# Kernel optimization log

Measured on AMD Instinct MI355X. Metric: run time of the kernel, lower is better.

## Reference

```python
import jax, jax.numpy as jnp
import numpy as np

N_NODES = 50000
N_EDGES = 800000
R = 3          # relations
D_IN = 96
D_HID = 96
D_OUT = 64


def setup_inputs() -> dict:
    key = jax.random.key(0)
    ks = jax.random.split(key, 10)
    s_in = 1.0 / np.sqrt(D_IN)
    s_hid = 1.0 / np.sqrt(D_HID)
    return {
        "x": jax.random.normal(ks[0], (N_NODES, D_IN), jnp.float32),
        "src": jax.random.randint(ks[1], (R, N_EDGES), 0, N_NODES, jnp.int32),
        "dst": jax.random.randint(ks[2], (R, N_EDGES), 0, N_NODES, jnp.int32),
        "Ws1": jax.random.normal(ks[3], (R, D_IN, D_HID), jnp.float32) * s_in,
        "Wn1": jax.random.normal(ks[4], (R, D_IN, D_HID), jnp.float32) * s_in,
        "b1": jnp.zeros((R, D_HID), jnp.float32),
        "Ws2": jax.random.normal(ks[5], (R, D_HID, D_OUT), jnp.float32) * s_hid,
        "Wn2": jax.random.normal(ks[6], (R, D_HID, D_OUT), jnp.float32) * s_hid,
        "b2": jnp.zeros((R, D_OUT), jnp.float32),
    }


def reference(x, src, dst, Ws1, Wn1, b1, Ws2, Wn2, b2):
    N = x.shape[0]
    # in-degree per relation, clamped to 1 (DGL zero-in-degree convention)
    deg = jax.vmap(lambda d: jax.ops.segment_sum(
        jnp.ones(d.shape[0], x.dtype), d, num_segments=N))(dst)        # [R, N]
    inv_deg = (1.0 / jnp.maximum(deg, 1.0))[..., None]                 # [R, N, 1]

    def sage_layer(h, Ws, Wn, b):
        # gather src feats, mean-aggregate onto dst, per relation
        neigh = jax.vmap(lambda s, d: jax.ops.segment_sum(
            h[s], d, num_segments=N))(src, dst) * inv_deg              # [R, N, Din]
        out = jnp.tanh(
            jnp.einsum('nd,rdh->rnh', h, Ws)
            + jnp.einsum('rnd,rdh->rnh', neigh, Wn)
            + b[:, None, :])                                           # [R, N, H]
        return out.mean(axis=0)  # HeteroGraphConv aggregate='mean'

    h1 = sage_layer(x, Ws1, Wn1, b1)
    return sage_layer(h1, Ws2, Wn2, b2)
```

## Files before the change

kernel.cpp:

```cpp
#include <hip/hip_runtime.h>
#include <hip/hip_bf16.h>

constexpr int NN   = 50000;
constexpr int NE   = 800000;
constexpr int NR   = 3;
constexpr int DIN  = 96;
constexpr int DH   = 96;
constexpr int DOUT = 64;
constexpr int SLOT = 48;
constexpr int ZROW = NN;

constexpr float QS_X   = 127.0f / 5.5f;
constexpr float STEP_X = 5.5f / 127.0f;
constexpr float STEP_H = 1.0f / 127.0f;

constexpr int NBUCK   = 196;
constexpr int LCAP    = 56;
constexpr int P1B     = 256;
constexpr int CHUNK   = NE / P1B;
constexpr int BSTRIDE = 3200;
constexpr int LSTRIDE = 200;

constexpr int SCAT_BLKS = NR * P1B;
constexpr int CONV_BLKS = (NN * 96 + 4095) / 4096;
constexpr int WT_ELEMS  = 2 * NR * DIN * DH + 2 * NR * DH * DOUT;
constexpr int WT_BLKS   = (WT_ELEMS + 511) / 512;
constexpr int PREP_GRID = SCAT_BLKS + CONV_BLKS + WT_BLKS;

typedef __attribute__((ext_vector_type(8))) short bf16x8;
typedef __attribute__((ext_vector_type(4))) float f32x4;
typedef __attribute__((ext_vector_type(4))) unsigned int uint4v;

__device__ __forceinline__ unsigned short f2b(float f) {
    unsigned int u = __float_as_uint(f);
    u += 0x7fffu + ((u >> 16) & 1u);
    return (unsigned short)(u >> 16);
}
__device__ __forceinline__ unsigned int pack2(float lo, float hi) {
    return (unsigned int)f2b(lo) | ((unsigned int)f2b(hi) << 16);
}
__device__ __forceinline__ unsigned int q8u(float f, float s) {
    int v = (int)lrintf(f * s);
    v = v < -127 ? -127 : (v > 127 ? 127 : v);
    return (unsigned int)(v + 128);
}

struct __align__(4) U3 { unsigned int x, y, z; };

__global__ __launch_bounds__(512)
void prep_kernel(const int* __restrict__ src,
                 const int* __restrict__ dst,
                 unsigned int* __restrict__ gbuck,
                 int* __restrict__ glofs,
                 const float* __restrict__ x,
                 unsigned short* __restrict__ xb,
                 unsigned char* __restrict__ xq,
                 const float* __restrict__ Ws1, const float* __restrict__ Wn1,
                 const float* __restrict__ Ws2, const float* __restrict__ Wn2,
                 unsigned short* __restrict__ wt)
{
    __shared__ unsigned int lbuf[NBUCK][LCAP];
    __shared__ int lcnt[NBUCK];
    __shared__ int sa[256], sb[256];
    __shared__ int lofs[NBUCK + 1];

    const int bid = blockIdx.x;
    const int tid = threadIdx.x;

    if (bid < SCAT_BLKS) {
        const int r = bid >> 8, c = bid & 255;
        for (int i = tid; i < NBUCK; i += 512) lcnt[i] = 0;
        __syncthreads();

        const int* sr = src + (size_t)r * NE + (size_t)c * CHUNK;
        const int* dr = dst + (size_t)r * NE + (size_t)c * CHUNK;
        for (int i = tid; i < CHUNK; i += 512) {
            int d = dr[i];
            int s = sr[i];
            int b = d >> 8;
            int pos = atomicAdd(&lcnt[b], 1);
            if (pos < LCAP)
                lbuf[b][pos] = ((unsigned int)(d & 255) << 16) | (unsigned int)s;
        }
        __syncthreads();

        if (tid < 256)
            sa[tid] = (tid < NBUCK) ? min(lcnt[tid], LCAP) : 0;
        __syncthreads();
        int* cur = sa; int* nxt = sb;
        for (int st = 1; st < 256; st <<= 1) {
            if (tid < 256) {
                int v = cur[tid];
                if (tid >= st) v += cur[tid - st];
                nxt[tid] = v;
            }
            __syncthreads();
            int* t2 = cur; cur = nxt; nxt = t2;
        }
        if (tid == 0) lofs[0] = 0;
        if (tid < NBUCK) lofs[tid + 1] = cur[tid];
        __syncthreads();

        if (tid < NBUCK + 1) glofs[(size_t)bid * LSTRIDE + tid] = lofs[tid];

        const int w = tid >> 6, l = tid & 63;
        unsigned int* gb = gbuck + (size_t)bid * BSTRIDE;
        for (int b = w; b < NBUCK; b += 8) {
            int cnt = min(lcnt[b], LCAP);
            if (l < cnt) gb[lofs[b] + l] = lbuf[b][l];
        }
    } else if (bid < SCAT_BLKS + CONV_BLKS) {
        const int rb = bid - SCAT_BLKS;
        if (rb == 0) {
            if (tid < 48) {
                unsigned int* z = reinterpret_cast<unsigned int*>(xb + (size_t)ZROW * 96);
                z[tid] = 0u;
            } else if (tid >= 64 && tid < 88) {
                reinterpret_cast<unsigned int*>(xq + (size_t)ZROW * 96)[tid - 64] = 0x80808080u;
            }
        }
        int i = (rb * 512 + tid) * 8;
        if (i < NN * 96) {
            float4 a = *reinterpret_cast<const float4*>(x + i);
            float4 b = *reinterpret_cast<const float4*>(x + i + 4);
            uint4 o;
            o.x = pack2(a.x, a.y);
            o.y = pack2(a.z, a.w);
            o.z = pack2(b.x, b.y);
            o.w = pack2(b.z, b.w);
            *reinterpret_cast<uint4*>(xb + i) = o;
            unsigned int qlo = q8u(a.x, QS_X) | (q8u(a.y, QS_X) << 8)
                             | (q8u(a.z, QS_X) << 16) | (q8u(a.w, QS_X) << 24);
            unsigned int qhi = q8u(b.x, QS_X) | (q8u(b.y, QS_X) << 8)
                             | (q8u(b.z, QS_X) << 16) | (q8u(b.w, QS_X) << 24);
            unsigned int* q = reinterpret_cast<unsigned int*>(xq + i);
            q[0] = qlo;
            q[1] = qhi;
        }
    } else {
        int g = (bid - SCAT_BLKS - CONV_BLKS) * 512 + tid;
        if (g < WT_ELEMS) {
            constexpr int SZ1 = NR * DIN * DH;
            constexpr int SZ2 = NR * DH * DOUT;
            const float* in;
            int idx, KD, ND;
            if (g < SZ1)                { in = Ws1; idx = g;                 KD = DIN; ND = DH; }
            else if (g < 2 * SZ1)       { in = Wn1; idx = g - SZ1;           KD = DIN; ND = DH; }
            else if (g < 2 * SZ1 + SZ2) { in = Ws2; idx = g - 2 * SZ1;       KD = DH;  ND = DOUT; }
            else                        { in = Wn2; idx = g - 2 * SZ1 - SZ2; KD = DH;  ND = DOUT; }
            int k = idx % KD;
            int rn = idx / KD;
            int n = rn % ND;
            int r = rn / ND;
            wt[g] = f2b(in[((size_t)r * KD + k) * ND + n]);
        }
    }
}

__global__ __launch_bounds__(512)
void bin_build_kernel(const unsigned int* __restrict__ gbuck,
                      const int* __restrict__ glofs,
                      unsigned short* __restrict__ slots,
                      int* __restrict__ deg)
{
    __shared__ unsigned short lslot[256][SLOT];
    __shared__ int lcnt[256];

    const int rb = blockIdx.x;
    const int r  = rb / NBUCK, b = rb - r * NBUCK;
    const int nbase = b * 256;
    int nb = NN - nbase; if (nb > 256) nb = 256;
    const int tid = threadIdx.x;

    unsigned int* ls32i = reinterpret_cast<unsigned int*>(&lslot[0][0]);
    for (int i = tid; i < 256 * SLOT / 2; i += 512) ls32i[i] = 0xC350C350u;
    for (int i = tid; i < 256; i += 512) lcnt[i] = 0;
    __syncthreads();

    const int blk  = tid >> 1;
    const int half = tid & 1;
    const int gblk = r * P1B + blk;
    int o0 = glofs[(size_t)gblk * LSTRIDE + b];
    int o1 = glofs[(size_t)gblk * LSTRIDE + b + 1];
    const unsigned int* run = gbuck + (size_t)gblk * BSTRIDE + o0;
    int cnt = o1 - o0;
    for (int i = half; i < cnt; i += 2) {
        unsigned int e = run[i];
        int nl = e >> 16;
        int pos = atomicAdd(&lcnt[nl], 1);
        if (pos < SLOT) lslot[nl][pos] = (unsigned short)(e & 0xffffu);
    }
    __syncthreads();

    for (int j = tid; j < nb; j += 512) deg[r * NN + nbase + j] = lcnt[j];

    const unsigned int* ls32 = reinterpret_cast<const unsigned int*>(&lslot[0][0]);
    unsigned int* gs32 = reinterpret_cast<unsigned int*>(
        slots + ((size_t)r * NN + nbase) * SLOT);
    const int tot = nb * (SLOT / 2);
    for (int i = tid; i < tot; i += 512) gs32[i] = ls32[i];
}

__global__ __launch_bounds__(256)
void agg_q8_kernel(const unsigned char* __restrict__ Hq,
                   const unsigned short* __restrict__ slots,
                   const int* __restrict__ deg,
                   unsigned int* __restrict__ aggb,
                   float step)
{
    int gid = blockIdx.x * 256 + threadIdx.x;
    int grp = gid >> 3, t = gid & 7;
    if (grp >= NR * NN) return;
    const uint4v* sl4 = reinterpret_cast<const uint4v*>(slots + (size_t)grp * SLOT);
    int e = deg[grp];
    if (e > SLOT) e = SLOT;

    uint4v iv0 = __builtin_nontemporal_load(sl4 + 0);
    uint4v iv1 = __builtin_nontemporal_load(sl4 + 1);
    uint4v iv2 = __builtin_nontemporal_load(sl4 + 2);
    uint4v iv3 = __builtin_nontemporal_load(sl4 + 3);

    const unsigned char* Tb = Hq + 12 * t;
    unsigned int l0 = 0, h0 = 0, l1 = 0, h1 = 0, l2 = 0, h2 = 0;
    const unsigned int M = 0x00FF00FFu;

#define DO8Q(V)                                                                \
    {                                                                          \
        unsigned int i0 = (V).x & 0xffffu, i1 = (V).x >> 16;                   \
        unsigned int i2 = (V).y & 0xffffu, i3 = (V).y >> 16;                   \
        unsigned int i4 = (V).z & 0xffffu, i5 = (V).z >> 16;                   \
        unsigned int i6 = (V).w & 0xffffu, i7 = (V).w >> 16;                   \
        U3 g0 = *reinterpret_cast<const U3*>(Tb + (size_t)i0 * 96);            \
        U3 g1 = *reinterpret_cast<const U3*>(Tb + (size_t)i1 * 96);            \
        U3 g2 = *reinterpret_cast<const U3*>(Tb + (size_t)i2 * 96);            \
        U3 g3 = *reinterpret_cast<const U3*>(Tb + (size_t)i3 * 96);            \
        U3 g4 = *reinterpret_cast<const U3*>(Tb + (size_t)i4 * 96);            \
        U3 g5 = *reinterpret_cast<const U3*>(Tb + (size_t)i5 * 96);            \
        U3 g6 = *reinterpret_cast<const U3*>(Tb + (size_t)i6 * 96);            \
        U3 g7 = *reinterpret_cast<const U3*>(Tb + (size_t)i7 * 96);            \
        l0 += g0.x & M; h0 += (g0.x >> 8) & M;                                 \
        l1 += g0.y & M; h1 += (g0.y >> 8) & M;                                 \
        l2 += g0.z & M; h2 += (g0.z >> 8) & M;                                 \
        l0 += g1.x & M; h0 += (g1.x >> 8) & M;                                 \
        l1 += g1.y & M; h1 += (g1.y >> 8) & M;                                 \
        l2 += g1.z & M; h2 += (g1.z >> 8) & M;                                 \
        l0 += g2.x & M; h0 += (g2.x >> 8) & M;                                 \
        l1 += g2.y & M; h1 += (g2.y >> 8) & M;                                 \
        l2 += g2.z & M; h2 += (g2.z >> 8) & M;                                 \
        l0 += g3.x & M; h0 += (g3.x >> 8) & M;                                 \
        l1 += g3.y & M; h1 += (g3.y >> 8) & M;                                 \
        l2 += g3.z & M; h2 += (g3.z >> 8) & M;                                 \
        l0 += g4.x & M; h0 += (g4.x >> 8) & M;                                 \
        l1 += g4.y & M; h1 += (g4.y >> 8) & M;                                 \
        l2 += g4.z & M; h2 += (g4.z >> 8) & M;                                 \
        l0 += g5.x & M; h0 += (g5.x >> 8) & M;                                 \
        l1 += g5.y & M; h1 += (g5.y >> 8) & M;                                 \
        l2 += g5.z & M; h2 += (g5.z >> 8) & M;                                 \
        l0 += g6.x & M; h0 += (g6.x >> 8) & M;                                 \
        l1 += g6.y & M; h1 += (g6.y >> 8) & M;                                 \
        l2 += g6.z & M; h2 += (g6.z >> 8) & M;                                 \
        l0 += g7.x & M; h0 += (g7.x >> 8) & M;                                 \
        l1 += g7.y & M; h1 += (g7.y >> 8) & M;                                 \
        l2 += g7.z & M; h2 += (g7.z >> 8) & M;                                 \
    }

    int nb8 = (e + 7) >> 3;
    if (nb8 > 0) DO8Q(iv0);
    if (nb8 > 1) DO8Q(iv1);
    if (nb8 > 2) DO8Q(iv2);
    if (nb8 > 3) DO8Q(iv3);
    for (int i = 32; i < e; i += 8) {
        uint4v v = __builtin_nontemporal_load(sl4 + (i >> 3));
        DO8Q(v);
    }
#undef DO8Q

    const int bias = 128 * 8 * nb8;
    const float inv = step / (float)(e > 0 ? e : 1);
    float f0  = (float)((int)(l0 & 0xFFFFu) - bias) * inv;
    float f1  = (float)((int)(h0 & 0xFFFFu) - bias) * inv;
    float f2  = (float)((int)(l0 >> 16)     - bias) * inv;
    float f3  = (float)((int)(h0 >> 16)     - bias) * inv;
    float f4  = (float)((int)(l1 & 0xFFFFu) - bias) * inv;
    float f5  = (float)((int)(h1 & 0xFFFFu) - bias) * inv;
    float f6  = (float)((int)(l1 >> 16)     - bias) * inv;
    float f7  = (float)((int)(h1 >> 16)     - bias) * inv;
    float f8  = (float)((int)(l2 & 0xFFFFu) - bias) * inv;
    float f9  = (float)((int)(h2 & 0xFFFFu) - bias) * inv;
    float f10 = (float)((int)(l2 >> 16)     - bias) * inv;
    float f11 = (float)((int)(h2 >> 16)     - bias) * inv;

    unsigned int* o = aggb + (size_t)grp * 48 + t * 6;
    o[0] = pack2(f0, f1);
    o[1] = pack2(f2, f3);
    o[2] = pack2(f4, f5);
    o[3] = pack2(f6, f7);
    o[4] = pack2(f8, f9);
    o[5] = pack2(f10, f11);
}

template <int NOUT, bool OUT16>
__global__ __launch_bounds__(256)
void mfma_layer_kernel(const unsigned short* Hb,
                       const unsigned short* __restrict__ aggb,
                       const unsigned short* __restrict__ Wts,
                       const unsigned short* __restrict__ Wtn,
                       const float* __restrict__ bias,
                       unsigned short* o16,
                       unsigned char* oq8,
                       float* __restrict__ o32)
{
    const int w    = threadIdx.x >> 6;
    const int l    = threadIdx.x & 63;
    const int n0   = blockIdx.x * 64 + w * 16;
    const int arow = l & 15, asel = l >> 4;
    int na = n0 + arow;
    if (na > NN - 1) na = NN - 1;

    bf16x8 ax[3], ag[NR][3];
    {
        const unsigned short* xr = Hb + (size_t)na * 96 + asel * 8;
        #pragma unroll
        for (int kb = 0; kb < 3; ++kb)
            ax[kb] = *reinterpret_cast<const bf16x8*>(xr + kb * 32);
        #pragma unroll
        for (int r = 0; r < NR; ++r) {
            const unsigned short* gr = aggb + ((size_t)r * NN + na) * 96 + asel * 8;
            #pragma unroll
            for (int kb = 0; kb < 3; ++kb)
                ag[r][kb] = *reinterpret_cast<const bf16x8*>(gr + kb * 32);
        }
    }

    constexpr int NC = NOUT / 16;
    #pragma unroll
    for (int c = 0; c < NC; ++c) {
        f32x4 acc[NR];
        #pragma unroll
        for (int r = 0; r < NR; ++r) acc[r] = (f32x4){0.f, 0.f, 0.f, 0.f};

        #pragma unroll
        for (int r = 0; r < NR; ++r) {
            const unsigned short* bs = Wts + ((size_t)r * NOUT + c * 16 + arow) * 96 + asel * 8;
            const unsigned short* bn = Wtn + ((size_t)r * NOUT + c * 16 + arow) * 96 + asel * 8;
            #pragma unroll
            for (int kb = 0; kb < 3; ++kb) {
                acc[r] = __builtin_amdgcn_mfma_f32_16x16x32_bf16(
                    ax[kb], *reinterpret_cast<const bf16x8*>(bs + kb * 32), acc[r], 0, 0, 0);
                acc[r] = __builtin_amdgcn_mfma_f32_16x16x32_bf16(
                    ag[r][kb], *reinterpret_cast<const bf16x8*>(bn + kb * 32), acc[r], 0, 0, 0);
            }
        }

        const int col = c * 16 + arow;
        const float b0 = bias[col];
        const float b1 = bias[NOUT + col];
        const float b2 = bias[2 * NOUT + col];
        #pragma unroll
        for (int j = 0; j < 4; ++j) {
            int node = n0 + asel * 4 + j;
            if (node < NN) {
                float v = (tanhf(acc[0][j] + b0) + tanhf(acc[1][j] + b1)
                         + tanhf(acc[2][j] + b2)) * (1.0f / 3.0f);
                if (OUT16) {
                    o16[(size_t)node * 96 + col] = f2b(v);
                    oq8[(size_t)node * 96 + col] = (unsigned char)q8u(v, 127.0f);
                } else {
                    o32[(size_t)node * DOUT + col] = v;
                }
            }
        }
    }
}

extern "C" void kernel_launch(void* const* d_in, const int* in_sizes, int n_in,
                              void* d_out, int out_size, void* d_ws, size_t ws_size,
                              hipStream_t stream)
{
    const float* x   = (const float*)d_in[0];
    const int*   src = (const int*)d_in[1];
    const int*   dst = (const int*)d_in[2];
    const float* Ws1 = (const float*)d_in[3];
    const float* Wn1 = (const float*)d_in[4];
    const float* b1  = (const float*)d_in[5];
    const float* Ws2 = (const float*)d_in[6];
    const float* Wn2 = (const float*)d_in[7];
    const float* b2  = (const float*)d_in[8];
    float* out = (float*)d_out;

    char* ws = (char*)d_ws;
    size_t o = 0;
    auto alloc = [&](size_t bytes) {
        size_t p = o;
        o += (bytes + 255) & ~(size_t)255;
        return p;
    };
    int* deg = (int*)(ws + alloc((size_t)NR * NN * 4));
    unsigned short* slots = (unsigned short*)(ws + alloc((size_t)NR * NN * SLOT * 2));
    unsigned short* xb = (unsigned short*)(ws + alloc((size_t)(NN + 1) * 96 * 2));
    unsigned char* xq = (unsigned char*)(ws + alloc((size_t)(NN + 1) * 96));
    char* aggregion = ws + alloc((size_t)NR * NN * 96 * 2);
    unsigned short* wt = (unsigned short*)(ws + alloc((size_t)WT_ELEMS * 2));
    unsigned short* wt1s = wt;
    unsigned short* wt1n = wt1s + NR * DIN * DH;
    unsigned short* wt2s = wt1n + NR * DIN * DH;
    unsigned short* wt2n = wt2s + NR * DH * DOUT;

    unsigned int* gbuck = (unsigned int*)aggregion;
    int* glofs = (int*)(aggregion + (size_t)NR * P1B * BSTRIDE * 4);
    unsigned short* aggb = (unsigned short*)aggregion;

    prep_kernel<<<PREP_GRID, 512, 0, stream>>>(
        src, dst, gbuck, glofs, x, xb, xq, Ws1, Wn1, Ws2, Wn2, wt);
    bin_build_kernel<<<NR * NBUCK, 512, 0, stream>>>(gbuck, glofs, slots, deg);

    constexpr int AGG_GRID  = (NR * NN * 8 + 255) / 256;
    constexpr int GEMM_GRID = (NN + 63) / 64;

    agg_q8_kernel<<<AGG_GRID, 256, 0, stream>>>(
        xq, slots, deg, (unsigned int*)aggb, STEP_X);
    mfma_layer_kernel<DH, true><<<GEMM_GRID, 256, 0, stream>>>(
        xb, aggb, wt1s, wt1n, b1, xb, xq, (float*)nullptr);

    agg_q8_kernel<<<AGG_GRID, 256, 0, stream>>>(
        xq, slots, deg, (unsigned int*)aggb, STEP_H);
    mfma_layer_kernel<DOUT, false><<<GEMM_GRID, 256, 0, stream>>>(
        xb, aggb, wt2s, wt2n, b2, (unsigned short*)nullptr, (unsigned char*)nullptr, out);
}
```

Baseline: 171.3 us.

## Split GEMM layer kernels across output column blocks with separate hidden buffers

The dense layer kernels now launch several blocks per 64-node tile, each computing a subset of output column chunks, which raises the number of blocks in flight. Because blocks of the first layer can no longer safely overwrite the input features in place, the hidden activations are written to new bf16 and int8 buffers, and the zero padding row is initialised for them. The cost is that every column block reloads the same input and aggregated rows, multiplying A-side memory traffic unless it hits in cache.

```diff
diff --git a/kernel.cpp b/kernel.cpp
--- a/kernel.cpp
+++ b/kernel.cpp
@@ -55,6 +55,8 @@
                  const float* __restrict__ x,
                  unsigned short* __restrict__ xb,
                  unsigned char* __restrict__ xq,
+                 unsigned short* __restrict__ h1b,
+                 unsigned char* __restrict__ h1q,
                  const float* __restrict__ Ws1, const float* __restrict__ Wn1,
                  const float* __restrict__ Ws2, const float* __restrict__ Wn2,
                  unsigned short* __restrict__ wt)
@@ -113,10 +115,13 @@
         const int rb = bid - SCAT_BLKS;
         if (rb == 0) {
             if (tid < 48) {
-                unsigned int* z = reinterpret_cast<unsigned int*>(xb + (size_t)ZROW * 96);
-                z[tid] = 0u;
-            } else if (tid >= 64 && tid < 88) {
-                reinterpret_cast<unsigned int*>(xq + (size_t)ZROW * 96)[tid - 64] = 0x80808080u;
+                reinterpret_cast<unsigned int*>(xb  + (size_t)ZROW * 96)[tid] = 0u;
+            } else if (tid >= 64 && tid < 112) {
+                reinterpret_cast<unsigned int*>(h1b + (size_t)ZROW * 96)[tid - 64] = 0u;
+            } else if (tid >= 128 && tid < 152) {
+                reinterpret_cast<unsigned int*>(xq  + (size_t)ZROW * 96)[tid - 128] = 0x80808080u;
+            } else if (tid >= 192 && tid < 216) {
+                reinterpret_cast<unsigned int*>(h1q + (size_t)ZROW * 96)[tid - 192] = 0x80808080u;
             }
         }
         int i = (rb * 512 + tid) * 8;
@@ -299,20 +304,22 @@
     o[5] = pack2(f10, f11);
 }
 
-template <int NOUT, bool OUT16>
+template <int NOUT, bool OUT16, int CSPLIT>
 __global__ __launch_bounds__(256)
-void mfma_layer_kernel(const unsigned short* Hb,
+void mfma_layer_kernel(const unsigned short* __restrict__ Hb,
                        const unsigned short* __restrict__ aggb,
                        const unsigned short* __restrict__ Wts,
                        const unsigned short* __restrict__ Wtn,
                        const float* __restrict__ bias,
-                       unsigned short* o16,
-                       unsigned char* oq8,
+                       unsigned short* __restrict__ o16,
+                       unsigned char* __restrict__ oq8,
                        float* __restrict__ o32)
 {
+    const int nb   = blockIdx.x / CSPLIT;
+    const int cblk = blockIdx.x - nb * CSPLIT;
     const int w    = threadIdx.x >> 6;
     const int l    = threadIdx.x & 63;
-    const int n0   = blockIdx.x * 64 + w * 16;
+    const int n0   = nb * 64 + w * 16;
     const int arow = l & 15, asel = l >> 4;
     int na = n0 + arow;
     if (na > NN - 1) na = NN - 1;
@@ -332,9 +339,11 @@
         }
     }
 
-    constexpr int NC = NOUT / 16;
+    constexpr int NC  = NOUT / 16;
+    constexpr int NCC = NC / CSPLIT;
     #pragma unroll
-    for (int c = 0; c < NC; ++c) {
+    for (int ci = 0; ci < NCC; ++ci) {
+        const int c = cblk * NCC + ci;
         f32x4 acc[NR];
         #pragma unroll
         for (int r = 0; r < NR; ++r) acc[r] = (f32x4){0.f, 0.f, 0.f, 0.f};
@@ -399,6 +408,8 @@
     unsigned short* slots = (unsigned short*)(ws + alloc((size_t)NR * NN * SLOT * 2));
     unsigned short* xb = (unsigned short*)(ws + alloc((size_t)(NN + 1) * 96 * 2));
     unsigned char* xq = (unsigned char*)(ws + alloc((size_t)(NN + 1) * 96));
+    unsigned short* h1b = (unsigned short*)(ws + alloc((size_t)(NN + 1) * 96 * 2));
+    unsigned char* h1q = (unsigned char*)(ws + alloc((size_t)(NN + 1) * 96));
     char* aggregion = ws + alloc((size_t)NR * NN * 96 * 2);
     unsigned short* wt = (unsigned short*)(ws + alloc((size_t)WT_ELEMS * 2));
     unsigned short* wt1s = wt;
@@ -411,19 +422,19 @@
     unsigned short* aggb = (unsigned short*)aggregion;
 
     prep_kernel<<<PREP_GRID, 512, 0, stream>>>(
-        src, dst, gbuck, glofs, x, xb, xq, Ws1, Wn1, Ws2, Wn2, wt);
+        src, dst, gbuck, glofs, x, xb, xq, h1b, h1q, Ws1, Wn1, Ws2, Wn2, wt);
     bin_build_kernel<<<NR * NBUCK, 512, 0, stream>>>(gbuck, glofs, slots, deg);
 
     constexpr int AGG_GRID  = (NR * NN * 8 + 255) / 256;
-    constexpr int GEMM_GRID = (NN + 63) / 64;
+    constexpr int NBLKN     = (NN + 63) / 64;
 
     agg_q8_kernel<<<AGG_GRID, 256, 0, stream>>>(
         xq, slots, deg, (unsigned int*)aggb, STEP_X);
-    mfma_layer_kernel<DH, true><<<GEMM_GRID, 256, 0, stream>>>(
-        xb, aggb, wt1s, wt1n, b1, xb, xq, (float*)nullptr);
+    mfma_layer_kernel<DH, true, 3><<<NBLKN * 3, 256, 0, stream>>>(
+        xb, aggb, wt1s, wt1n, b1, h1b, h1q, (float*)nullptr);
 
     agg_q8_kernel<<<AGG_GRID, 256, 0, stream>>>(
-        xq, slots, deg, (unsigned int*)aggb, STEP_H);
-    mfma_layer_kernel<DOUT, false><<<GEMM_GRID, 256, 0, stream>>>(
-        xb, aggb, wt2s, wt2n, b2, (unsigned short*)nullptr, (unsigned char*)nullptr, out);
-}
+        h1q, slots, deg, (unsigned int*)aggb, STEP_H);
+    mfma_layer_kernel<DOUT, false, 2><<<NBLKN * 2, 256, 0, stream>>>(
+        h1b, aggb, wt2s, wt2n, b2, (unsigned short*)nullptr, (unsigned char*)nullptr, out);
+}
```

After: 175.2 us. 1.02x slower.
